# Kernel tuning notes

Hardware: AMD Instinct MI355X
Metric: run time of the kernel (lower is better)

Reference implementation:

```python
import jax, jax.numpy as jnp
import numpy as np
from jax import lax

N_POINTS = 400000
WIDTH = 64  # 3 xyz + 61 payload features
STRIDE = 400


def setup_inputs() -> dict:
    key = jax.random.key(0)
    feats = jax.random.normal(key, (N_POINTS, WIDTH), dtype=jnp.float32)
    return {"feats": feats}


def _furthest_point_sampling(p, m):
    """Iterative FPS over p: [N, 3], returning m int32 indices.

    Mirrors pointops.furthestsampling: seed with index 0, maintain running
    min squared distance to the sampled set, pick argmax each step.
    """
    n = p.shape[0]
    init_dists = jnp.full((n,), 1e10, dtype=p.dtype)

    def step(carry, _):
        dists, last = carry
        # squared distance from every point to the most recently sampled point
        d = jnp.sum(jnp.square(p - p[last]), axis=-1)  # [N]
        dists = jnp.minimum(dists, d)
        nxt = jnp.argmax(dists).astype(jnp.int32)
        return (dists, nxt), nxt

    (_, _), rest = lax.scan(step, (init_dists, jnp.int32(0)), None, length=m - 1)
    return jnp.concatenate([jnp.zeros((1,), dtype=jnp.int32), rest])


def reference(feats):
    p = feats[:, :3]  # xyz coordinates; feats[:, 3:] are unused payload
    n = feats.shape[0]
    m = n // STRIDE  # n_o = [N // stride] for the single batch
    idx = _furthest_point_sampling(p, m)
    return idx
```

## Files before the change

kernel.cpp:

```cpp
#include <hip/hip_runtime.h>
#include <stdint.h>

#define N_POINTS   400000
#define WIDTH      64
#define M_SAMPLES  1000
#define NBLK       64
#define NTHR       512
#define NWAVE      (NTHR / 64)
#define NTOT       (NBLK * NTHR)
#define PPT        13
#define TAIL_GID   (N_POINTS - (PPT - 1) * NTOT)
#define EPAD       8
#define NREG       128
#define SLOT_WORDS (NREG * NBLK * EPAD)


__global__ void fps_init(unsigned long long* slot, int* out) {
    int t = blockIdx.x * blockDim.x + threadIdx.x;
    if (t < SLOT_WORDS) slot[t] = 0ull;
    if (t == 0) out[0] = 0;
}

template <int STAGES, int SRCLANE>
__device__ inline unsigned long long wave_scan_max_u64(unsigned long long key) {
    unsigned int lo = (unsigned int)key;
    unsigned int hi = (unsigned int)(key >> 32);
#define FPS_DPP_STAGE(CTRL)                                                     \
    {                                                                           \
        unsigned int nlo = (unsigned int)__builtin_amdgcn_update_dpp(           \
            (int)lo, (int)lo, CTRL, 0xf, 0xf, false);                           \
        unsigned int nhi = (unsigned int)__builtin_amdgcn_update_dpp(           \
            (int)hi, (int)hi, CTRL, 0xf, 0xf, false);                           \
        unsigned long long cand = ((unsigned long long)nhi << 32) | nlo;        \
        unsigned long long cur  = ((unsigned long long)hi  << 32) | lo;         \
        if (cand > cur) { lo = nlo; hi = nhi; }                                 \
    }
    if constexpr (STAGES > 0) FPS_DPP_STAGE(0x111)
    if constexpr (STAGES > 1) FPS_DPP_STAGE(0x112)
    if constexpr (STAGES > 2) FPS_DPP_STAGE(0x114)
    if constexpr (STAGES > 3) FPS_DPP_STAGE(0x118)
    if constexpr (STAGES > 4) FPS_DPP_STAGE(0x142)
    if constexpr (STAGES > 5) FPS_DPP_STAGE(0x143)
#undef FPS_DPP_STAGE
    unsigned int rlo = (unsigned int)__builtin_amdgcn_readlane((int)lo, SRCLANE);
    unsigned int rhi = (unsigned int)__builtin_amdgcn_readlane((int)hi, SRCLANE);
    return ((unsigned long long)rhi << 32) | rlo;
}

__global__ __launch_bounds__(NTHR)
void fps_main(const float* __restrict__ feats, int* __restrict__ out,
              unsigned long long* __restrict__ slot)
{
    const int tid  = threadIdx.x;
    const int bid  = blockIdx.x;
    const int lane = tid & 63;
    const int wid  = tid >> 6;
    const int gid  = bid * NTHR + tid;

    float px[PPT], py[PPT], pz[PPT], dd[PPT];
#pragma unroll
    for (int k = 0; k < PPT; k++) {
        int j = gid + k * NTOT;
        if (j < N_POINTS) {
            float4 v = *reinterpret_cast<const float4*>(feats + (size_t)j * WIDTH);
            px[k] = v.x; py[k] = v.y; pz[k] = v.z;
        } else {
            px[k] = 0.f; py[k] = 0.f; pz[k] = 0.f;
        }
        dd[k] = 1e10f;
    }

    __shared__ unsigned long long s_wmax[NWAVE];
    __shared__ float s_qx, s_qy, s_qz;

    float qx = feats[0];
    float qy = feats[1];
    float qz = feats[2];

    for (int i = 1; i < M_SAMPLES; i++) {
        const unsigned long long tg = (unsigned long long)(i & 255);
        unsigned long long* cur = slot + (size_t)((i - 1) & (NREG - 1)) * NBLK * EPAD;

        float bd = -1.0f;
        unsigned int bj = 0;
#pragma unroll
        for (int k = 0; k < PPT; k++) {
            int j = gid + k * NTOT;
            float dx = __fsub_rn(px[k], qx);
            float dy = __fsub_rn(py[k], qy);
            float dz = __fsub_rn(pz[k], qz);
            float d  = __fadd_rn(__fadd_rn(__fmul_rn(dx, dx), __fmul_rn(dy, dy)),
                                 __fmul_rn(dz, dz));
            float nd = fminf(dd[k], d);
            dd[k] = nd;
            bool upd = (nd > bd);
            if (k == PPT - 1) upd = upd && (gid < TAIL_GID);
            bd = upd ? nd : bd;
            bj = upd ? (unsigned int)j : bj;
        }
        unsigned long long key =
            ((unsigned long long)__float_as_uint(bd) << 32) |
            (tg << 19) |
            (unsigned long long)(N_POINTS - bj);

        unsigned long long wmax = wave_scan_max_u64<6, 63>(key);
        if (lane == 0) s_wmax[wid] = wmax;
        __syncthreads();

        if (wid == 0) {
            unsigned long long bk = (lane < NWAVE) ? s_wmax[lane] : 0ull;
            unsigned long long blockmax = wave_scan_max_u64<3, 7>(bk);
            if (lane == 0)
                __hip_atomic_store(&cur[(size_t)bid * EPAD], blockmax,
                                   __ATOMIC_RELAXED, __HIP_MEMORY_SCOPE_AGENT);

            const unsigned long long* lp = cur + (size_t)lane * EPAD;
            unsigned long long a, b, c, e;
            a = __hip_atomic_load(lp, __ATOMIC_RELAXED, __HIP_MEMORY_SCOPE_AGENT);
            b = __hip_atomic_load(lp, __ATOMIC_RELAXED, __HIP_MEMORY_SCOPE_AGENT);
            c = __hip_atomic_load(lp, __ATOMIC_RELAXED, __HIP_MEMORY_SCOPE_AGENT);
            for (;;) {
                if (((a >> 19) & 255ull) == tg) { e = a; break; }
                a = b; b = c;
                c = __hip_atomic_load(lp, __ATOMIC_RELAXED,
                                      __HIP_MEMORY_SCOPE_AGENT);
            }

            unsigned int widx = N_POINTS - (unsigned int)(e & 0x7FFFFull);
            float4 pv = *reinterpret_cast<const float4*>(feats + (size_t)widx * WIDTH);

            unsigned long long win = wave_scan_max_u64<6, 63>(e);

            if (e == win) {
                s_qx = pv.x; s_qy = pv.y; s_qz = pv.z;
                if (bid == 0) out[i] = (int)widx;
            }
        }
        __syncthreads();
        qx = s_qx; qy = s_qy; qz = s_qz;
    }
}

extern "C" void kernel_launch(void* const* d_in, const int* in_sizes, int n_in,
                              void* d_out, int out_size, void* d_ws, size_t ws_size,
                              hipStream_t stream) {
    const float* feats = (const float*)d_in[0];
    int* out = (int*)d_out;
    unsigned long long* slot = (unsigned long long*)d_ws;

    fps_init<<<(SLOT_WORDS + 255) / 256, 256, 0, stream>>>(slot, out);
    fps_main<<<NBLK, NTHR, 0, stream>>>(feats, out, slot);
}
```

Before: 2.423 ms.

## Carry winner coordinates through reductions and slots instead of reloading from feats

```diff
diff --git a/kernel.cpp b/kernel.cpp
--- a/kernel.cpp
+++ b/kernel.cpp
@@ -47,6 +47,39 @@
     return ((unsigned long long)rhi << 32) | rlo;
 }
 
+__device__ inline void row8_max_with_payload(
+    unsigned long long key, float x, float y, float z,
+    unsigned long long& okey, float& ox, float& oy, float& oz)
+{
+    unsigned int lo = (unsigned int)key, hi = (unsigned int)(key >> 32);
+#define FPS_DPPP(CTRL)                                                          \
+    {                                                                           \
+        unsigned int nlo = (unsigned int)__builtin_amdgcn_update_dpp(           \
+            (int)lo, (int)lo, CTRL, 0xf, 0xf, false);                           \
+        unsigned int nhi = (unsigned int)__builtin_amdgcn_update_dpp(           \
+            (int)hi, (int)hi, CTRL, 0xf, 0xf, false);                           \
+        float nx = __uint_as_float((unsigned int)__builtin_amdgcn_update_dpp(   \
+            (int)__float_as_uint(x), (int)__float_as_uint(x), CTRL, 0xf, 0xf, false)); \
+        float ny = __uint_as_float((unsigned int)__builtin_amdgcn_update_dpp(   \
+            (int)__float_as_uint(y), (int)__float_as_uint(y), CTRL, 0xf, 0xf, false)); \
+        float nz = __uint_as_float((unsigned int)__builtin_amdgcn_update_dpp(   \
+            (int)__float_as_uint(z), (int)__float_as_uint(z), CTRL, 0xf, 0xf, false)); \
+        unsigned long long cand = ((unsigned long long)nhi << 32) | nlo;        \
+        unsigned long long cur  = ((unsigned long long)hi  << 32) | lo;         \
+        if (cand > cur) { lo = nlo; hi = nhi; x = nx; y = ny; z = nz; }         \
+    }
+    FPS_DPPP(0x111)
+    FPS_DPPP(0x112)
+    FPS_DPPP(0x114)
+#undef FPS_DPPP
+    unsigned int rlo = (unsigned int)__builtin_amdgcn_readlane((int)lo, 7);
+    unsigned int rhi = (unsigned int)__builtin_amdgcn_readlane((int)hi, 7);
+    okey = ((unsigned long long)rhi << 32) | rlo;
+    ox = __uint_as_float((unsigned int)__builtin_amdgcn_readlane((int)__float_as_uint(x), 7));
+    oy = __uint_as_float((unsigned int)__builtin_amdgcn_readlane((int)__float_as_uint(y), 7));
+    oz = __uint_as_float((unsigned int)__builtin_amdgcn_readlane((int)__float_as_uint(z), 7));
+}
+
 __global__ __launch_bounds__(NTHR)
 void fps_main(const float* __restrict__ feats, int* __restrict__ out,
               unsigned long long* __restrict__ slot)
@@ -70,7 +103,8 @@
         dd[k] = 1e10f;
     }
 
-    __shared__ unsigned long long s_wmax[NWAVE];
+    __shared__ unsigned long long s_key[NWAVE];
+    __shared__ float s_x[NWAVE], s_y[NWAVE], s_z[NWAVE];
     __shared__ float s_qx, s_qy, s_qz;
 
     float qx = feats[0];
@@ -81,7 +115,7 @@
         const unsigned long long tg = (unsigned long long)(i & 255);
         unsigned long long* cur = slot + (size_t)((i - 1) & (NREG - 1)) * NBLK * EPAD;
 
-        float bd = -1.0f;
+        float bd = -1.0f, bx = 0.f, by = 0.f, bz = 0.f;
         unsigned int bj = 0;
 #pragma unroll
         for (int k = 0; k < PPT; k++) {
@@ -97,6 +131,9 @@
             if (k == PPT - 1) upd = upd && (gid < TAIL_GID);
             bd = upd ? nd : bd;
             bj = upd ? (unsigned int)j : bj;
+            bx = upd ? px[k] : bx;
+            by = upd ? py[k] : by;
+            bz = upd ? pz[k] : bz;
         }
         unsigned long long key =
             ((unsigned long long)__float_as_uint(bd) << 32) |
@@ -104,36 +141,47 @@
             (unsigned long long)(N_POINTS - bj);
 
         unsigned long long wmax = wave_scan_max_u64<6, 63>(key);
-        if (lane == 0) s_wmax[wid] = wmax;
+        if (key == wmax) {
+            s_key[wid] = wmax;
+            s_x[wid] = bx; s_y[wid] = by; s_z[wid] = bz;
+        }
         __syncthreads();
 
         if (wid == 0) {
-            unsigned long long bk = (lane < NWAVE) ? s_wmax[lane] : 0ull;
-            unsigned long long blockmax = wave_scan_max_u64<3, 7>(bk);
-            if (lane == 0)
-                __hip_atomic_store(&cur[(size_t)bid * EPAD], blockmax,
+            unsigned long long bk = (lane < NWAVE) ? s_key[lane] : 0ull;
+            float lx = (lane < NWAVE) ? s_x[lane] : 0.f;
+            float ly = (lane < NWAVE) ? s_y[lane] : 0.f;
+            float lz = (lane < NWAVE) ? s_z[lane] : 0.f;
+            unsigned long long blockkey; float wx, wy, wz;
+            row8_max_with_payload(bk, lx, ly, lz, blockkey, wx, wy, wz);
+
+            unsigned long long w =
+                (lane == 0) ? blockkey :
+                (lane == 1) ? (((unsigned long long)__float_as_uint(wx) << 32) | tg) :
+                (lane == 2) ? (((unsigned long long)__float_as_uint(wy) << 32) | tg) :
+                              (((unsigned long long)__float_as_uint(wz) << 32) | tg);
+            if (lane < 4)
+                __hip_atomic_store(&cur[(size_t)bid * EPAD + lane], w,
                                    __ATOMIC_RELAXED, __HIP_MEMORY_SCOPE_AGENT);
 
             const unsigned long long* lp = cur + (size_t)lane * EPAD;
-            unsigned long long a, b, c, e;
-            a = __hip_atomic_load(lp, __ATOMIC_RELAXED, __HIP_MEMORY_SCOPE_AGENT);
-            b = __hip_atomic_load(lp, __ATOMIC_RELAXED, __HIP_MEMORY_SCOPE_AGENT);
-            c = __hip_atomic_load(lp, __ATOMIC_RELAXED, __HIP_MEMORY_SCOPE_AGENT);
+            unsigned long long w0, w1, w2, w3;
             for (;;) {
-                if (((a >> 19) & 255ull) == tg) { e = a; break; }
-                a = b; b = c;
-                c = __hip_atomic_load(lp, __ATOMIC_RELAXED,
-                                      __HIP_MEMORY_SCOPE_AGENT);
+                w0 = __hip_atomic_load(lp + 0, __ATOMIC_RELAXED, __HIP_MEMORY_SCOPE_AGENT);
+                w1 = __hip_atomic_load(lp + 1, __ATOMIC_RELAXED, __HIP_MEMORY_SCOPE_AGENT);
+                w2 = __hip_atomic_load(lp + 2, __ATOMIC_RELAXED, __HIP_MEMORY_SCOPE_AGENT);
+                w3 = __hip_atomic_load(lp + 3, __ATOMIC_RELAXED, __HIP_MEMORY_SCOPE_AGENT);
+                if ((((w0 >> 19) & 255ull) == tg) & ((w1 & 255ull) == tg) &
+                    ((w2 & 255ull) == tg) & ((w3 & 255ull) == tg)) break;
             }
 
-            unsigned int widx = N_POINTS - (unsigned int)(e & 0x7FFFFull);
-            float4 pv = *reinterpret_cast<const float4*>(feats + (size_t)widx * WIDTH);
-
-            unsigned long long win = wave_scan_max_u64<6, 63>(e);
-
-            if (e == win) {
-                s_qx = pv.x; s_qy = pv.y; s_qz = pv.z;
-                if (bid == 0) out[i] = (int)widx;
+            unsigned long long win = wave_scan_max_u64<6, 63>(w0);
+            if (w0 == win) {
+                s_qx = __uint_as_float((unsigned int)(w1 >> 32));
+                s_qy = __uint_as_float((unsigned int)(w2 >> 32));
+                s_qz = __uint_as_float((unsigned int)(w3 >> 32));
+                if (bid == 0)
+                    out[i] = (int)(N_POINTS - (unsigned int)(w0 & 0x7FFFFull));
             }
         }
         __syncthreads();
```

After: 2.478 ms. +2.3%, slower.
